# Kernel tuning notes

Hardware: AMD Instinct MI355X
Metric: run time of the kernel (lower is better)

Reference implementation:

```python
import jax, jax.numpy as jnp
import numpy as np

B, T, C, N = 4, 12, 64, 10000
H = 64            # d_inner (GRU hidden)
L = 2             # num_layers
NE = 2000         # number of static hyperedges
NNZ = 80000       # incidence list length
TOPK = 10         # HGCNADP_topk
DE = 16           # HGCNADP_embed_dims
RATE = 0.5        # hyperedge_rate (blend static vs adaptive)


def setup_inputs() -> dict:
    key = jax.random.key(0)
    ks = jax.random.split(key, 10)
    scale = 0.05
    x = jax.random.normal(ks[0], (B, T, C, N), jnp.float32)
    node_idx = jax.random.randint(ks[1], (NNZ,), 0, N, jnp.int32)
    edge_idx = jax.random.randint(ks[2], (NNZ,), 0, NE, jnp.int32)
    hyperedge_index = jnp.stack([node_idx, edge_idx])  # (2, NNZ)
    node_embs = jax.random.normal(ks[3], (L, N, DE), jnp.float32) * 0.1
    W_zr = jax.random.normal(ks[4], (L, C + H, 2 * H), jnp.float32) * scale
    b_zr = jnp.zeros((L, 2 * H), jnp.float32)
    W_c = jax.random.normal(ks[5], (L, C + H, H), jnp.float32) * scale
    b_c = jnp.zeros((L, H), jnp.float32)
    W_out = jax.random.normal(ks[6], (L, H, C), jnp.float32) * scale
    b_out = jnp.zeros((L, C), jnp.float32)
    return {"x": x, "hyperedge_index": hyperedge_index, "node_embs": node_embs,
            "W_zr": W_zr, "b_zr": b_zr, "W_c": W_c, "b_c": b_c,
            "W_out": W_out, "b_out": b_out}


def reference(x, hyperedge_index, node_embs, W_zr, b_zr, W_c, b_c, W_out, b_out):
    # x: (B, T, C, N). Dropout is identity (eval mode).
    node_idx = hyperedge_index[0]
    edge_idx = hyperedge_index[1]
    edge_deg = jnp.zeros((NE,), x.dtype).at[edge_idx].add(1.0)
    inv_e = 1.0 / jnp.maximum(edge_deg, 1.0)
    node_deg = jnp.zeros((N,), x.dtype).at[node_idx].add(1.0)
    inv_n = 1.0 / jnp.maximum(node_deg, 1.0)

    def conv(f, topk_idx, topk_w):
        # f: (B, N, D). Static hypergraph pass: node -> hyperedge -> node.
        msg = jnp.take(f, node_idx, axis=1)                       # (B, NNZ, D)
        eagg = jnp.zeros((f.shape[0], NE, f.shape[2]), f.dtype).at[:, edge_idx].add(msg)
        eagg = eagg * inv_e[None, :, None]                        # (B, NE, D)
        stat = jnp.zeros_like(f).at[:, node_idx].add(jnp.take(eagg, edge_idx, axis=1))
        stat = stat * inv_n[None, :, None]                        # (B, N, D)
        # Adaptive top-k hyperedge aggregation (softmax-weighted neighbor sum).
        adp = jnp.einsum('bnkd,nk->bnd', jnp.take(f, topk_idx, axis=1), topk_w)
        return RATE * stat + (1.0 - RATE) * adp

    out = x
    for l in range(L):
        xl = out.transpose(0, 1, 3, 2)                            # (B, T, N, C)
        E = node_embs[l]
        scores = jax.nn.relu(E @ E.T)                             # (N, N)
        vals, idx = jax.lax.top_k(scores, TOPK)                   # (N, K)
        w = jax.nn.softmax(vals, axis=-1)
        Wz, bz = W_zr[l], b_zr[l]
        Wc_, bc_ = W_c[l], b_c[l]
        Wo, bo = W_out[l], b_out[l]

        def step(h, x_t):
            zr = jax.nn.sigmoid(conv(jnp.concatenate([x_t, h], -1), idx, w) @ Wz + bz)
            z, r = jnp.split(zr, 2, axis=-1)
            c = jnp.tanh(conv(jnp.concatenate([x_t, r * h], -1), idx, w) @ Wc_ + bc_)
            h_new = z * h + (1.0 - z) * c
            return h_new, h_new @ Wo + bo

        h0 = jnp.zeros((out.shape[0], N, H), x.dtype)
        _, ys = jax.lax.scan(step, h0, xl.transpose(1, 0, 2, 3))  # ys: (T, B, N, C)
        out = out + ys.transpose(1, 0, 3, 2)                      # residual, back to (B,T,C,N)
    return out
```

## Files before the change

kernel.cpp:

```cpp
#include <hip/hip_runtime.h>
#include <hip/hip_fp16.h>
#include <cstdio>

#define BB 4
#define TT 12
#define CC 64
#define NN 10000
#define HH 64
#define LL 2
#define NEDGE 2000
#define NNZT 80000
#define KTOP 10
#define DEMB 16
#define BT (BB*TT)
#define TOPK_BLKS 1250
#define TRN_BLKS 30048

typedef long long ll;
typedef unsigned long long u64;
typedef unsigned int u32;
typedef unsigned short ushort;

typedef short bf16x8 __attribute__((ext_vector_type(8)));
typedef float f32x4 __attribute__((ext_vector_type(4)));

__device__ __forceinline__ void up8(const uint4 v, float* f) {
  const __half2* p = reinterpret_cast<const __half2*>(&v);
  float2 t0 = __half22float2(p[0]);
  float2 t1 = __half22float2(p[1]);
  float2 t2 = __half22float2(p[2]);
  float2 t3 = __half22float2(p[3]);
  f[0]=t0.x; f[1]=t0.y; f[2]=t1.x; f[3]=t1.y;
  f[4]=t2.x; f[5]=t2.y; f[6]=t3.x; f[7]=t3.y;
}
__device__ __forceinline__ uint4 pk8(const float* f) {
  __half2 h0 = __floats2half2_rn(f[0], f[1]);
  __half2 h1 = __floats2half2_rn(f[2], f[3]);
  __half2 h2 = __floats2half2_rn(f[4], f[5]);
  __half2 h3 = __floats2half2_rn(f[6], f[7]);
  uint4 r;
  r.x = *reinterpret_cast<unsigned*>(&h0);
  r.y = *reinterpret_cast<unsigned*>(&h1);
  r.z = *reinterpret_cast<unsigned*>(&h2);
  r.w = *reinterpret_cast<unsigned*>(&h3);
  return r;
}
__device__ __forceinline__ ushort f2bf(float x) {
  u32 u = __float_as_uint(x);
  u32 r = u + 0x7FFFu + ((u >> 16) & 1u);
  return (ushort)(r >> 16);
}
__device__ __forceinline__ uint4 pk8bf(const float* f) {
  uint4 r;
  r.x = (u32)f2bf(f[0]) | ((u32)f2bf(f[1])<<16);
  r.y = (u32)f2bf(f[2]) | ((u32)f2bf(f[3])<<16);
  r.z = (u32)f2bf(f[4]) | ((u32)f2bf(f[5])<<16);
  r.w = (u32)f2bf(f[6]) | ((u32)f2bf(f[7])<<16);
  return r;
}

__global__ void deg_kernel(const int* __restrict__ nidx, const int* __restrict__ eidx,
                           int* __restrict__ ndeg, int* __restrict__ edeg) {
  int i = blockIdx.x*256 + threadIdx.x;
  if (i < NNZT) { atomicAdd(&ndeg[nidx[i]],1); atomicAdd(&edeg[eidx[i]],1); }
}

__global__ void exscan_kernel(const int* __restrict__ cnt, int* __restrict__ off, int n) {
  __shared__ int part[256];
  int tid = threadIdx.x;
  int chunk = (n + 255)/256;
  int lo = tid*chunk, hi = min(lo+chunk, n);
  int s = 0;
  for (int i=lo; i<hi; ++i) s += cnt[i];
  part[tid]=s; __syncthreads();
  if (tid==0){ int acc=0; for(int i=0;i<256;++i){int v=part[i];part[i]=acc;acc+=v;} off[n]=acc; }
  __syncthreads();
  int acc = part[tid];
  for (int i=lo; i<hi; ++i){ off[i]=acc; acc+=cnt[i]; }
}

__global__ void fill_csr_kernel(const int* __restrict__ nidx, const int* __restrict__ eidx,
                                const int* __restrict__ noff, const int* __restrict__ eoff,
                                int* __restrict__ ncur, int* __restrict__ ecur,
                                int* __restrict__ node_edges, int* __restrict__ edge_nodes) {
  int i = blockIdx.x*256 + threadIdx.x;
  if (i >= NNZT) return;
  int n = nidx[i], e = eidx[i];
  int pn = atomicAdd(&ncur[n],1);
  node_edges[noff[n]+pn] = e;
  int pe = atomicAdd(&ecur[e],1);
  edge_nodes[eoff[e]+pe] = n;
}

__global__ void invdeg_kernel(const int* __restrict__ ndeg, const int* __restrict__ edeg,
                              float* __restrict__ inv_n, float* __restrict__ inv_e) {
  int i = blockIdx.x*256+threadIdx.x;
  if (i < NN) inv_n[i] = 1.0f/fmaxf((float)ndeg[i],1.0f);
  if (i < NEDGE) inv_e[i] = 1.0f/fmaxf((float)edeg[i],1.0f);
}

__global__ void prep_w_kernel(const float* __restrict__ W_zr, const float* __restrict__ W_c,
                              const float* __restrict__ W_o,
                              short* __restrict__ Wz_swb, short* __restrict__ Wc_swb,
                              short* __restrict__ Wo_swb) {
  int l = blockIdx.y;
  const float* Wz = W_zr + (size_t)l*128*128;
  const float* Wc = W_c  + (size_t)l*128*64;
  const float* Wo = W_o  + (size_t)l*64*64;
  short* Wz_sw = Wz_swb + (size_t)l*16384;
  short* Wc_sw = Wc_swb + (size_t)l*8192;
  short* Wo_sw = Wo_swb + (size_t)l*4096;
  int idx = blockIdx.x*256 + threadIdx.x;
  if (idx < 16384) {
    int i = idx&7, lane = (idx>>3)&63, kk = (idx>>9)&3, tc = idx>>11;
    int k = kk*32 + (lane>>4)*8 + i, col = tc*16 + (lane&15);
    Wz_sw[idx] = (short)f2bf(Wz[k*128+col]);
  }
  if (idx < 8192) {
    int i = idx&7, lane = (idx>>3)&63, kk = (idx>>9)&3, tc = idx>>11;
    int k = kk*32 + (lane>>4)*8 + i, col = tc*16 + (lane&15);
    Wc_sw[idx] = (short)f2bf(Wc[k*64+col]);
  }
  if (idx < 4096) {
    int i = idx&7, lane = (idx>>3)&63, kk = (idx>>9)&1, tc = idx>>10;
    int k = kk*32 + (lane>>4)*8 + i, col = tc*16 + (lane&15);
    Wo_sw[idx] = (short)f2bf(Wo[k*64+col]);
  }
}

__device__ __forceinline__ u64 sortstep(u64 X, int j, bool dir, int lane) {
  u64 p = __shfl_xor(X, j);
  bool lower = ((lane & j) == 0);
  bool keep_min = (dir == lower);
  bool xlt = (X < p);
  u64 mn = xlt ? X : p;
  u64 mx = xlt ? p : X;
  return keep_min ? mn : mx;
}

__device__ __forceinline__ void reselect(u64* bq, u64& thr, int& cnt, int lane) {
  int tot = 10 + cnt;
  u64 A = (lane < tot)      ? bq[lane]      : 0ull;
  u64 B = (lane + 64 < tot) ? bq[lane + 64] : 0ull;
  for (int k = 2; k <= 32; k <<= 1) {
    for (int j = k >> 1; j >= 1; j >>= 1) {
      bool dir = ((lane & k) == 0);
      A = sortstep(A, j, dir, lane);
      B = sortstep(B, j, dir, lane);
    }
  }
  for (int j = 32; j >= 1; j >>= 1) {
    A = sortstep(A, j, true,  lane);
    B = sortstep(B, j, false, lane);
  }
  {
    bool lt = (A < B);
    u64 mn = lt ? A : B, mx = lt ? B : A;
    A = mn; B = mx;
  }
  for (int j = 32; j >= 1; j >>= 1) {
    A = sortstep(A, j, true, lane);
    B = sortstep(B, j, true, lane);
  }
  if (lane >= 54) bq[63 - lane] = B;
  thr = __shfl(B, 54);
  cnt = 0;
}

__device__ void topk_body(int layer, int qb, char* smem,
                          const float* __restrict__ embs, int2* __restrict__ tkc_b) {
  u64 (*buf)[128] = (u64(*)[128])smem;
  const float* E = embs + (ll)layer*NN*DEMB;
  int2* tkc = tkc_b + (ll)layer*NN*KTOP;
  int tid = threadIdx.x;
  int wv = tid >> 6, lane = tid & 63;
  int qbase = qb*16 + wv*4;
  const float4* E4 = (const float4*)E;
  float4 q[4][4];
  #pragma unroll
  for (int u=0;u<4;++u) {
    int n = qbase + u;
    #pragma unroll
    for (int j=0;j<4;++j) q[u][j] = E4[(ll)n*4 + j];
  }
  u64 thr[4] = {0,0,0,0};
  float thrf[4] = {0.f,0.f,0.f,0.f};
  int cnt[4] = {0,0,0,0};
  buf[tid>>4][tid&15] = 0ull;
  for (int cb=0; cb<NN; cb+=64) {
    int cand = cb + lane;
    bool valid = (cand < NN);
    int ca = valid ? cand : 0;
    float4 a0 = E4[(ll)ca*4], a1 = E4[(ll)ca*4+1], a2 = E4[(ll)ca*4+2], a3 = E4[(ll)ca*4+3];
    u64 low = (u64)(0x00FFFFFFu - (unsigned)cand);
    float sv[4];
    #pragma unroll
    for (int u=0;u<4;++u) {
      float dot = q[u][0].x*a0.x + q[u][0].y*a0.y + q[u][0].z*a0.z + q[u][0].w*a0.w
                + q[u][1].x*a1.x + q[u][1].y*a1.y + q[u][1].z*a1.z + q[u][1].w*a1.w
                + q[u][2].x*a2.x + q[u][2].y*a2.y + q[u][2].z*a2.z + q[u][2].w*a2.w
                + q[u][3].x*a3.x + q[u][3].y*a3.y + q[u][3].z*a3.z + q[u][3].w*a3.w;
      float s = fmaxf(dot, 0.f);
      sv[u] = valid ? s : -1.f;
    }
    #pragma unroll
    for (int u=0;u<4;++u) {
      u64 mask = __ballot(sv[u] >= thrf[u]);
      if (mask) {
        if (sv[u] >= thrf[u]) {
          u64 key = ((u64)__float_as_uint(sv[u]) << 32) | low;
          int myofs = (int)__popcll(mask & ((1ull<<lane)-1ull));
          buf[wv*4+u][10 + cnt[u] + myofs] = key;
        }
        cnt[u] += (int)__popcll(mask);
        if (cnt[u] >= 40) {
          reselect(&buf[wv*4+u][0], thr[u], cnt[u], lane);
          thrf[u] = __uint_as_float((u32)(thr[u] >> 32));
        }
      }
    }
  }
  #pragma unroll
  for (int u=0;u<4;++u) {
    u64* bq = &buf[wv*4+u][0];
    if (cnt[u] > 0) reselect(bq, thr[u], cnt[u], lane);
    u64 k10 = (lane < 10) ? bq[lane] : 0ull;
    float v = __uint_as_float((unsigned)(k10 >> 32));
    int idx = 0x00FFFFFF - (int)(k10 & 0xFFFFFFFFull);
    float v0 = __shfl(v, 0);
    float e = (lane < 10) ? expf(v - v0) : 0.f;
    float s = e;
    for (int o=1;o<16;o<<=1) s += __shfl_xor(s, o);
    if (lane < 10) {
      int n = qbase + u;
      tkc[n*KTOP + lane] = make_int2(idx, __float_as_int(e / s));
    }
  }
}

__device__ void transpose_body(int tb, char* smem,
                               const float* __restrict__ src, __half* __restrict__ dst) {
  float (*tile)[33] = (float(*)[33])smem;
  int tid = threadIdx.x;
  int tx = tid & 31, ty = tid >> 5;
  int bt = tb / 626;
  int rem = tb % 626;
  int n0 = (rem % 313)*32, c0 = (rem/313)*32;
  for (int i=ty; i<32; i+=8) {
    int c = c0+i, nn = n0+tx;
    tile[i][tx] = (nn<NN)? src[((ll)bt*CC + c)*NN + nn] : 0.0f;
  }
  __syncthreads();
  for (int i=ty; i<32; i+=8) {
    int nn = n0+i, c = c0+tx;
    if (nn<NN) dst[((ll)bt*NN+nn)*64 + c] = __float2half_rn(tile[tx][i]);
  }
}

__global__ void __launch_bounds__(256) mega1_kernel(const float* __restrict__ embs,
                                                    int2* __restrict__ tkc,
                                                    const float* __restrict__ x,
                                                    __half* __restrict__ xt) {
  __shared__ __align__(16) char smem[16384];
  int bid = blockIdx.x;
  if (bid < TOPK_BLKS) topk_body(bid/625, bid%625, smem, embs, tkc);
  else transpose_body(bid - TOPK_BLKS, smem, x, xt);
}

__global__ void transpose_kernel(const float* __restrict__ src, __half* __restrict__ dst) {
  __shared__ __align__(16) char smem[4352];
  int tb = (blockIdx.z*626) + blockIdx.y*313 + blockIdx.x;
  transpose_body(tb, smem, src, dst);
}

__global__ void __launch_bounds__(256) edge_agg_kernel(
    const uint4* __restrict__ f8, uint4* __restrict__ eagg8,
    const int* __restrict__ eoff, const int* __restrict__ enodes,
    const float* __restrict__ inv_e) {
  __shared__ int en_s[1088];
  __shared__ int jo_s[17];
  int tid = threadIdx.x;
  int e0 = blockIdx.x*16;
  int s = blockIdx.y;
  if (tid < 17) jo_s[tid] = eoff[e0 + tid];
  __syncthreads();
  int jb0 = jo_s[0], cnt = jo_s[16] - jb0;
  bool stg = (cnt <= 1088);
  if (stg) for (int i = tid; i < cnt; i += 256) en_s[i] = enodes[jb0 + i];
  __syncthreads();
  int esub = tid>>4;
  int e = e0 + esub;
  int hsel = (tid>>3)&1;
  int lane8 = tid&7;
  int j0 = jo_s[esub] - jb0, j1 = jo_s[esub+1] - jb0;
  const uint4* fb = f8 + (ll)s*NN*8;
  float acc[8] = {0,0,0,0,0,0,0,0};
  for (int j = j0 + hsel; j < j1; j += 2) {
    int node = stg ? en_s[j] : enodes[jb0+j];
    float t[8]; up8(fb[(ll)node*8 + lane8], t);
    #pragma unroll
    for (int q=0;q<8;++q) acc[q] += t[q];
  }
  #pragma unroll
  for (int q=0;q<8;++q) acc[q] += __shfl_xor(acc[q], 8);
  if (hsel == 0) {
    float sc = inv_e[e];
    #pragma unroll
    for (int q=0;q<8;++q) acc[q] *= sc;
    eagg8[((ll)s*NEDGE+e)*8 + lane8] = pk8(acc);
  }
}

__global__ void __launch_bounds__(256) conv_x_kernel(
    const uint4* __restrict__ xt8, const uint4* __restrict__ eagg8,
    const int* __restrict__ noff, const int* __restrict__ nedges,
    const float* __restrict__ inv_n,
    const int2* __restrict__ tkc,
    uint4* __restrict__ cx8) {
  __shared__ int tki_s[32][KTOP];
  __shared__ float tkw_s[32][KTOP];
  __shared__ int ne_s[640];
  __shared__ int no_s[33];
  int tid = threadIdx.x; int s = blockIdx.y; int n0 = blockIdx.x*32;
  if (tid < 33) no_s[tid] = noff[min(n0 + tid, NN)];
  for (int i=tid; i<32*KTOP; i+=256) {
    int r=i/KTOP, k=i%KTOP; int n = n0+r;
    int2 p = (n<NN)? tkc[n*KTOP+k] : make_int2(0,0);
    tki_s[r][k] = p.x;
    tkw_s[r][k] = __int_as_float(p.y);
  }
  __syncthreads();
  int jb0 = no_s[0], cnt = no_s[32] - jb0;
  bool stg = (cnt <= 640);
  if (stg) for (int i=tid; i<cnt; i+=256) ne_s[i] = nedges[jb0+i];
  __syncthreads();
  int row = tid>>3, lane8 = tid&7;
  int n = n0 + row;
  if (n >= NN) return;
  float stv[8] = {0,0,0,0,0,0,0,0};
  const uint4* eb = eagg8 + (ll)s*NEDGE*8;
  int j0 = no_s[row] - jb0, j1 = no_s[row+1] - jb0;
  for (int j=j0;j<j1;++j) {
    int eidx = stg ? ne_s[j] : nedges[jb0+j];
    float t[8]; up8(eb[(ll)eidx*8 + lane8], t);
    #pragma unroll
    for (int q=0;q<8;++q) stv[q] += t[q];
  }
  float sc = 0.5f*inv_n[n];
  float adv[8] = {0,0,0,0,0,0,0,0};
  const uint4* xb = xt8 + (ll)s*NN*8;
  #pragma unroll
  for (int k=0;k<KTOP;++k) {
    float w = tkw_s[row][k];
    float t[8]; up8(xb[(ll)tki_s[row][k]*8 + lane8], t);
    #pragma unroll
    for (int q=0;q<8;++q) adv[q] += w*t[q];
  }
  float r8[8];
  #pragma unroll
  for (int q=0;q<8;++q) r8[q] = sc*stv[q] + 0.5f*adv[q];
  cx8[((ll)s*NN+n)*8+lane8] = pk8bf(r8);
}

__global__ void __launch_bounds__(256) step0_kernel(
    const uint4* __restrict__ cx8,
    const short* __restrict__ Wz_sw, const float* __restrict__ bz,
    const short* __restrict__ Wc_sw, const float* __restrict__ bc,
    const short* __restrict__ Wo_sw, const float* __restrict__ bo,
    __half* __restrict__ h, float* __restrict__ out) {
  __shared__ __align__(16) short in_bf[32][72];
  __shared__ __align__(16) short hn[32][72];
  __shared__ __align__(16) float yt[64][36];
  int tid = threadIdx.x;
  int b = blockIdx.y; int n0 = blockIdx.x*32;
  int bt = b*TT;
  {
    int row = tid>>3, lane8 = tid&7;
    int n = n0 + row;
    uint4 cxv4 = make_uint4(0,0,0,0);
    if (n < NN) cxv4 = cx8[((ll)bt*NN + n)*8 + lane8];
    *(uint4*)&in_bf[row][lane8*8] = cxv4;
  }
  __syncthreads();
  int wv = tid>>6, lane = tid&63;
  int m = lane&15, g = lane>>4;
  #pragma unroll
  for (int q=0;q<2;++q) {
    int T = wv + 4*q;
    int tr = T>>2, tc = T&3;
    f32x4 az = {0.f,0.f,0.f,0.f};
    f32x4 ac = {0.f,0.f,0.f,0.f};
    #pragma unroll
    for (int kk=0;kk<2;++kk) {
      bf16x8 a = *(const bf16x8*)&in_bf[tr*16 + m][kk*32 + g*8];
      bf16x8 bwz = *(const bf16x8*)&Wz_sw[((tc*4+kk)*64 + lane)*8];
      bf16x8 bwc = *(const bf16x8*)&Wc_sw[((tc*4+kk)*64 + lane)*8];
      az = __builtin_amdgcn_mfma_f32_16x16x32_bf16(a, bwz, az, 0, 0, 0);
      ac = __builtin_amdgcn_mfma_f32_16x16x32_bf16(a, bwc, ac, 0, 0, 0);
    }
    int col = tc*16 + m;
    float bzv = bz[col], bcv = bc[col];
    #pragma unroll
    for (int r=0;r<4;++r) {
      int row = tr*16 + g*4 + r;
      int n = n0 + row;
      float z = 1.0f/(1.0f+expf(-(az[r]+bzv)));
      float cval = tanhf(ac[r]+bcv);
      float hnew = (1.0f-z)*cval;
      if (n < NN) h[((ll)b*NN+n)*64+col] = __float2half_rn(hnew);
      hn[row][col] = (short)f2bf(hnew);
    }
  }
  __syncthreads();
  #pragma unroll
  for (int q=0;q<2;++q) {
    int T = wv + 4*q;
    int tr = T>>2, tc = T&3;
    f32x4 acc = {0.f,0.f,0.f,0.f};
    #pragma unroll
    for (int kk=0;kk<2;++kk) {
      bf16x8 a = *(const bf16x8*)&hn[tr*16 + m][kk*32 + g*8];
      bf16x8 bw = *(const bf16x8*)&Wo_sw[((tc*2+kk)*64 + lane)*8];
      acc = __builtin_amdgcn_mfma_f32_16x16x32_bf16(a, bw, acc, 0, 0, 0);
    }
    int col = tc*16 + m;
    float bias = bo[col];
    #pragma unroll
    for (int r=0;r<4;++r) {
      int row = tr*16 + g*4 + r;
      yt[col][row] = acc[r] + bias;
    }
  }
  __syncthreads();
  #pragma unroll
  for (int kk=0;kk<2;++kk) {
    int slot = tid + kk*256;
    int col = slot>>3, q = slot&7;
    int n = n0 + q*4;
    if (n < NN) {
      float4 y = *(const float4*)&yt[col][q*4];
      float4* dst = (float4*)&out[((ll)bt*64+col)*NN + n];
      float4 cur = *dst;
      cur.x += y.x; cur.y += y.y; cur.z += y.z; cur.w += y.w;
      *dst = cur;
    }
  }
}

__global__ void __launch_bounds__(256) step_zr_kernel(
    const uint4* __restrict__ h8, const uint4* __restrict__ cx8,
    const uint4* __restrict__ eagg8,
    const short* __restrict__ Wz_sw, const float* __restrict__ bz,
    const int* __restrict__ noff, const int* __restrict__ nedges,
    const float* __restrict__ inv_n,
    const int2* __restrict__ tkc,
    const __half* __restrict__ hs,
    __half* __restrict__ rh, __half* __restrict__ zout, int t) {
  __shared__ __align__(16) short in_bf[32][136];
  __shared__ int tki_s[32][KTOP];
  __shared__ float tkw_s[32][KTOP];
  __shared__ int ne_s[640];
  __shared__ int no_s[33];
  int tid = threadIdx.x;
  int b = blockIdx.y; int n0 = blockIdx.x*32;
  int bt = b*TT + t;
  if (tid < 33) no_s[tid] = noff[min(n0 + tid, NN)];
  for (int i=tid; i<32*KTOP; i+=256) {
    int r=i/KTOP, k=i%KTOP; int n=n0+r;
    int2 p = (n<NN)? tkc[n*KTOP+k] : make_int2(0,0);
    tki_s[r][k] = p.x;
    tkw_s[r][k] = __int_as_float(p.y);
  }
  __syncthreads();
  int jb0 = no_s[0], ecnt = no_s[32] - jb0;
  bool stg = (ecnt <= 640);
  if (stg) for (int i=tid; i<ecnt; i+=256) ne_s[i] = nedges[jb0+i];
  __syncthreads();
  {
    int row = tid>>3, lane8 = tid&7;
    int n = n0 + row;
    uint4 cxv4 = make_uint4(0,0,0,0);
    float chv[8] = {0,0,0,0,0,0,0,0};
    if (n < NN) {
      cxv4 = cx8[((ll)bt*NN + n)*8 + lane8];
      float stv[8] = {0,0,0,0,0,0,0,0};
      int j0 = no_s[row] - jb0, j1 = no_s[row+1] - jb0;
      const uint4* eb = eagg8 + (ll)b*NEDGE*8;
      for (int j=j0;j<j1;++j) {
        int eidx = stg ? ne_s[j] : nedges[jb0+j];
        float t8[8]; up8(eb[(ll)eidx*8 + lane8], t8);
        #pragma unroll
        for (int q=0;q<8;++q) stv[q] += t8[q];
      }
      float sc = 0.5f*inv_n[n];
      const uint4* hb = h8 + (ll)b*NN*8;
      float adv[8] = {0,0,0,0,0,0,0,0};
      #pragma unroll
      for (int k=0;k<KTOP;++k) {
        float w = tkw_s[row][k];
        float t8[8]; up8(hb[(ll)tki_s[row][k]*8 + lane8], t8);
        #pragma unroll
        for (int q=0;q<8;++q) adv[q] += w*t8[q];
      }
      #pragma unroll
      for (int q=0;q<8;++q) chv[q] = sc*stv[q] + 0.5f*adv[q];
    }
    *(uint4*)&in_bf[row][lane8*8]    = cxv4;
    *(uint4*)&in_bf[row][64+lane8*8] = pk8bf(chv);
  }
  __syncthreads();
  int wv = tid>>6, lane = tid&63;
  int m = lane&15, g = lane>>4;
  #pragma unroll
  for (int q=0;q<4;++q) {
    int T = wv*4 + q;
    int tr = T>>3, tc = T&7;
    f32x4 acc = {0.f,0.f,0.f,0.f};
    #pragma unroll
    for (int kk=0;kk<4;++kk) {
      bf16x8 a = *(const bf16x8*)&in_bf[tr*16 + m][kk*32 + g*8];
      bf16x8 bf = *(const bf16x8*)&Wz_sw[((tc*4+kk)*64 + lane)*8];
      acc = __builtin_amdgcn_mfma_f32_16x16x32_bf16(a, bf, acc, 0, 0, 0);
    }
    int col = tc*16 + m;
    float bias = bz[col];
    #pragma unroll
    for (int r=0;r<4;++r) {
      int row = tr*16 + g*4 + r;
      int n = n0 + row;
      if (n < NN) {
        float v = 1.0f/(1.0f+expf(-(acc[r]+bias)));
        if (col < 64) zout[((ll)b*NN+n)*64+col] = __float2half_rn(v);
        else {
          int c = col-64;
          float hv = __half2float(hs[((ll)b*NN+n)*64+c]);
          rh[((ll)b*NN+n)*64+c] = __float2half_rn(v*hv);
        }
      }
    }
  }
}

__global__ void __launch_bounds__(256) step_hy_kernel(
    const uint4* __restrict__ rh8, const uint4* __restrict__ cx8,
    const uint4* __restrict__ eagg8,
    const short* __restrict__ Wc_sw, const float* __restrict__ bc,
    const short* __restrict__ Wo_sw, const float* __restrict__ bo,
    const int* __restrict__ noff, const int* __restrict__ nedges,
    const float* __restrict__ inv_n,
    const int2* __restrict__ tkc,
    const __half* __restrict__ zbuf, __half* __restrict__ h,
    float* __restrict__ out, int t) {
  __shared__ __align__(16) short in_bf[32][136];
  __shared__ __align__(16) short hn[32][72];
  __shared__ __align__(16) float yt[64][36];
  __shared__ int tki_s[32][KTOP];
  __shared__ float tkw_s[32][KTOP];
  __shared__ int ne_s[640];
  __shared__ int no_s[33];
  int tid = threadIdx.x;
  int b = blockIdx.y; int n0 = blockIdx.x*32;
  int bt = b*TT + t;
  if (tid < 33) no_s[tid] = noff[min(n0 + tid, NN)];
  for (int i=tid; i<32*KTOP; i+=256) {
    int r=i/KTOP, k=i%KTOP; int n=n0+r;
    int2 p = (n<NN)? tkc[n*KTOP+k] : make_int2(0,0);
    tki_s[r][k] = p.x;
    tkw_s[r][k] = __int_as_float(p.y);
  }
  __syncthreads();
  int jb0 = no_s[0], ecnt = no_s[32] - jb0;
  bool stg = (ecnt <= 640);
  if (stg) for (int i=tid; i<ecnt; i+=256) ne_s[i] = nedges[jb0+i];
  __syncthreads();
  {
    int row = tid>>3, lane8 = tid&7;
    int n = n0 + row;
    uint4 cxv4 = make_uint4(0,0,0,0);
    float chv[8] = {0,0,0,0,0,0,0,0};
    if (n < NN) {
      cxv4 = cx8[((ll)bt*NN + n)*8 + lane8];
      float stv[8] = {0,0,0,0,0,0,0,0};
      int j0 = no_s[row] - jb0, j1 = no_s[row+1] - jb0;
      const uint4* eb = eagg8 + (ll)b*NEDGE*8;
      for (int j=j0;j<j1;++j) {
        int eidx = stg ? ne_s[j] : nedges[jb0+j];
        float t8[8]; up8(eb[(ll)eidx*8 + lane8], t8);
        #pragma unroll
        for (int q=0;q<8;++q) stv[q] += t8[q];
      }
      float sc = 0.5f*inv_n[n];
      const uint4* rb = rh8 + (ll)b*NN*8;
      float adv[8] = {0,0,0,0,0,0,0,0};
      #pragma unroll
      for (int k=0;k<KTOP;++k) {
        float w = tkw_s[row][k];
        float t8[8]; up8(rb[(ll)tki_s[row][k]*8 + lane8], t8);
        #pragma unroll
        for (int q=0;q<8;++q) adv[q] += w*t8[q];
      }
      #pragma unroll
      for (int q=0;q<8;++q) chv[q] = sc*stv[q] + 0.5f*adv[q];
    }
    *(uint4*)&in_bf[row][lane8*8]    = cxv4;
    *(uint4*)&in_bf[row][64+lane8*8] = pk8bf(chv);
  }
  __syncthreads();
  int wv = tid>>6, lane = tid&63;
  int m = lane&15, g = lane>>4;
  #pragma unroll
  for (int q=0;q<2;++q) {
    int T = wv + 4*q;
    int tr = T>>2, tc = T&3;
    f32x4 acc = {0.f,0.f,0.f,0.f};
    #pragma unroll
    for (int kk=0;kk<4;++kk) {
      bf16x8 a = *(const bf16x8*)&in_bf[tr*16 + m][kk*32 + g*8];
      bf16x8 bf = *(const bf16x8*)&Wc_sw[((tc*4+kk)*64 + lane)*8];
      acc = __builtin_amdgcn_mfma_f32_16x16x32_bf16(a, bf, acc, 0, 0, 0);
    }
    int col = tc*16 + m;
    float bias = bc[col];
    #pragma unroll
    for (int r=0;r<4;++r) {
      int row = tr*16 + g*4 + r;
      int n = n0 + row;
      float hnew = 0.0f;
      if (n < NN) {
        float cval = tanhf(acc[r]+bias);
        float z = __half2float(zbuf[((ll)b*NN+n)*64+col]);
        float hv = __half2float(h[((ll)b*NN+n)*64+col]);
        hnew = z*hv + (1.0f-z)*cval;
        h[((ll)b*NN+n)*64+col] = __float2half_rn(hnew);
      }
      hn[row][col] = (short)f2bf(hnew);
    }
  }
  __syncthreads();
  #pragma unroll
  for (int q=0;q<2;++q) {
    int T = wv + 4*q;
    int tr = T>>2, tc = T&3;
    f32x4 acc = {0.f,0.f,0.f,0.f};
    #pragma unroll
    for (int kk=0;kk<2;++kk) {
      bf16x8 a = *(const bf16x8*)&hn[tr*16 + m][kk*32 + g*8];
      bf16x8 bf = *(const bf16x8*)&Wo_sw[((tc*2+kk)*64 + lane)*8];
      acc = __builtin_amdgcn_mfma_f32_16x16x32_bf16(a, bf, acc, 0, 0, 0);
    }
    int col = tc*16 + m;
    float bias = bo[col];
    #pragma unroll
    for (int r=0;r<4;++r) {
      int row = tr*16 + g*4 + r;
      yt[col][row] = acc[r] + bias;
    }
  }
  __syncthreads();
  #pragma unroll
  for (int kk=0;kk<2;++kk) {
    int slot = tid + kk*256;
    int col = slot>>3, q = slot&7;
    int n = n0 + q*4;
    if (n < NN) {
      float4 y = *(const float4*)&yt[col][q*4];
      float4* dst = (float4*)&out[((ll)bt*64+col)*NN + n];
      float4 cur = *dst;
      cur.x += y.x; cur.y += y.y; cur.z += y.z; cur.w += y.w;
      *dst = cur;
    }
  }
}

extern "C" void kernel_launch(void* const* d_in, const int* in_sizes, int n_in,
                              void* d_out, int out_size, void* d_ws, size_t ws_size,
                              hipStream_t stream) {
  const float* x    = (const float*)d_in[0];
  const int*  hidx  = (const int*)d_in[1];
  const float* embs = (const float*)d_in[2];
  const float* W_zr = (const float*)d_in[3];
  const float* b_zr = (const float*)d_in[4];
  const float* W_c  = (const float*)d_in[5];
  const float* b_c  = (const float*)d_in[6];
  const float* W_out= (const float*)d_in[7];
  const float* b_out= (const float*)d_in[8];
  const int* node_idx = hidx;
  const int* edge_idx = hidx + NNZT;

  char* ws = (char*)d_ws;
  size_t off = 0;
  auto alloc = [&](size_t bytes) -> void* {
    void* p = ws + off; off += (bytes + 255) & ~(size_t)255; return p;
  };
  __half* xt    = (__half*)alloc((size_t)BT*NN*64*2);
  __half* cx    = (__half*)alloc((size_t)BT*NN*64*2);
  __half* eaggx = (__half*)alloc((size_t)BT*NEDGE*64*2);
  __half* eaggh = (__half*)alloc((size_t)BB*NEDGE*64*2);
  __half* hbuf  = (__half*)alloc((size_t)BB*NN*64*2);
  __half* rhbuf = (__half*)alloc((size_t)BB*NN*64*2);
  __half* zbuf  = (__half*)alloc((size_t)BB*NN*64*2);
  short* Wz_sw = (short*)alloc((size_t)LL*16384*2);
  short* Wc_sw = (short*)alloc((size_t)LL*8192*2);
  short* Wo_sw = (short*)alloc((size_t)LL*4096*2);
  int2* tkc    = (int2*)alloc((size_t)LL*NN*KTOP*8);
  float* inv_e = (float*)alloc(NEDGE*4);
  float* inv_n = (float*)alloc(NN*4);
  int* ndeg    = (int*)alloc(NN*4);
  int* edeg    = (int*)alloc(NEDGE*4);
  int* noff    = (int*)alloc((NN+1)*4);
  int* eoff    = (int*)alloc((NEDGE+1)*4);
  int* ncur    = (int*)alloc(NN*4);
  int* ecur    = (int*)alloc(NEDGE*4);
  int* nedges  = (int*)alloc(NNZT*4);
  int* enodes  = (int*)alloc(NNZT*4);
  if (off > ws_size) {
    fprintf(stderr, "kernel_launch: ws too small, need %zu have %zu\n", off, ws_size);
    return;
  }

  hipMemcpyAsync(d_out, x, (size_t)BB*TT*CC*NN*4, hipMemcpyDeviceToDevice, stream);

  hipMemsetAsync(ndeg, 0, NN*4, stream);
  hipMemsetAsync(edeg, 0, NEDGE*4, stream);
  hipMemsetAsync(ncur, 0, NN*4, stream);
  hipMemsetAsync(ecur, 0, NEDGE*4, stream);
  deg_kernel<<<(NNZT+255)/256,256,0,stream>>>(node_idx, edge_idx, ndeg, edeg);
  exscan_kernel<<<1,256,0,stream>>>(ndeg, noff, NN);
  exscan_kernel<<<1,256,0,stream>>>(edeg, eoff, NEDGE);
  fill_csr_kernel<<<(NNZT+255)/256,256,0,stream>>>(node_idx, edge_idx, noff, eoff,
                                                   ncur, ecur, nedges, enodes);
  invdeg_kernel<<<(NN+255)/256,256,0,stream>>>(ndeg, edeg, inv_n, inv_e);

  prep_w_kernel<<<dim3(64,LL),256,0,stream>>>(W_zr, W_c, W_out, Wz_sw, Wc_sw, Wo_sw);
  float* outp = (float*)d_out;
  mega1_kernel<<<TOPK_BLKS + TRN_BLKS,256,0,stream>>>(embs, tkc, outp, xt);

  for (int l=0; l<LL; ++l) {
    const short* Wzs = Wz_sw + (size_t)l*16384;
    const short* Wcs = Wc_sw + (size_t)l*8192;
    const short* Wos = Wo_sw + (size_t)l*4096;
    const float* bz = b_zr + l*128;
    const float* bc = b_c + l*64;
    const float* bo = b_out + l*64;
    const int2* tkcl = tkc + (size_t)l*NN*KTOP;
    if (l > 0)
      transpose_kernel<<<dim3(313, 2, BT), 256, 0, stream>>>(outp, xt);
    edge_agg_kernel<<<dim3(125, BT),256,0,stream>>>(
        (const uint4*)xt, (uint4*)eaggx, eoff, enodes, inv_e);
    conv_x_kernel<<<dim3(313, BT),256,0,stream>>>(
        (const uint4*)xt, (const uint4*)eaggx, noff, nedges, inv_n, tkcl, (uint4*)cx);
    step0_kernel<<<dim3(313, BB),256,0,stream>>>(
        (const uint4*)cx, Wzs, bz, Wcs, bc, Wos, bo, hbuf, outp);
    for (int t=1; t<TT; ++t) {
      edge_agg_kernel<<<dim3(125, BB),256,0,stream>>>(
          (const uint4*)hbuf, (uint4*)eaggh, eoff, enodes, inv_e);
      step_zr_kernel<<<dim3(313, BB),256,0,stream>>>(
          (const uint4*)hbuf, (const uint4*)cx, (const uint4*)eaggh, Wzs, bz,
          noff, nedges, inv_n, tkcl, hbuf, rhbuf, zbuf, t);
      edge_agg_kernel<<<dim3(125, BB),256,0,stream>>>(
          (const uint4*)rhbuf, (uint4*)eaggh, eoff, enodes, inv_e);
      step_hy_kernel<<<dim3(313, BB),256,0,stream>>>(
          (const uint4*)rhbuf, (const uint4*)cx, (const uint4*)eaggh, Wcs, bc, Wos, bo,
          noff, nedges, inv_n, tkcl, zbuf, hbuf, outp, t);
    }
  }
}
```

Baseline: 2.354 ms.

## Halve node tile in recurrent step kernels and split edge aggregation finer

The per-timestep GRU kernels (step0, step_zr, step_hy) now process 16 nodes per block instead of 32, doubling the grid to 625 blocks per batch. This exposes more parallelism in the small B=4 recurrent launches, and since 10000 is divisible by 16 the bounds checks can be dropped. A new edge aggregation kernel handles 8 edges per block with 4 partial sums per edge, used for the hidden-state passes, to raise occupancy. The top-k scan also prefetches the next candidate embeddings one iteration ahead to hide load latency. In exchange, only half the threads do the gather work in the step kernels, and the per-edge reduction needs an extra shuffle.

```diff
diff --git a/kernel.cpp b/kernel.cpp
--- a/kernel.cpp
+++ b/kernel.cpp
@@ -15,6 +15,7 @@
 #define BT (BB*TT)
 #define TOPK_BLKS 1250
 #define TRN_BLKS 30048
+#define NB16 625
 
 typedef long long ll;
 typedef unsigned long long u64;
@@ -187,11 +188,21 @@
   float thrf[4] = {0.f,0.f,0.f,0.f};
   int cnt[4] = {0,0,0,0};
   buf[tid>>4][tid&15] = 0ull;
+  float4 a0,a1,a2,a3;
+  {
+    int ca = (lane < NN) ? lane : 0;
+    a0=E4[(ll)ca*4]; a1=E4[(ll)ca*4+1]; a2=E4[(ll)ca*4+2]; a3=E4[(ll)ca*4+3];
+  }
   for (int cb=0; cb<NN; cb+=64) {
+    float4 b0,b1,b2,b3;
+    int ncb = cb + 64;
+    if (ncb < NN) {
+      int cand2 = ncb + lane;
+      int ca2 = (cand2 < NN) ? cand2 : 0;
+      b0=E4[(ll)ca2*4]; b1=E4[(ll)ca2*4+1]; b2=E4[(ll)ca2*4+2]; b3=E4[(ll)ca2*4+3];
+    }
     int cand = cb + lane;
     bool valid = (cand < NN);
-    int ca = valid ? cand : 0;
-    float4 a0 = E4[(ll)ca*4], a1 = E4[(ll)ca*4+1], a2 = E4[(ll)ca*4+2], a3 = E4[(ll)ca*4+3];
     u64 low = (u64)(0x00FFFFFFu - (unsigned)cand);
     float sv[4];
     #pragma unroll
@@ -219,6 +230,7 @@
         }
       }
     }
+    a0=b0; a1=b1; a2=b2; a3=b3;
   }
   #pragma unroll
   for (int u=0;u<4;++u) {
@@ -304,6 +316,46 @@
   #pragma unroll
   for (int q=0;q<8;++q) acc[q] += __shfl_xor(acc[q], 8);
   if (hsel == 0) {
+    float sc = inv_e[e];
+    #pragma unroll
+    for (int q=0;q<8;++q) acc[q] *= sc;
+    eagg8[((ll)s*NEDGE+e)*8 + lane8] = pk8(acc);
+  }
+}
+
+__global__ void __launch_bounds__(256) edge_agg8_kernel(
+    const uint4* __restrict__ f8, uint4* __restrict__ eagg8,
+    const int* __restrict__ eoff, const int* __restrict__ enodes,
+    const float* __restrict__ inv_e) {
+  __shared__ int en_s[576];
+  __shared__ int jo_s[9];
+  int tid = threadIdx.x;
+  int e0 = blockIdx.x*8;
+  int s = blockIdx.y;
+  if (tid < 9) jo_s[tid] = eoff[e0 + tid];
+  __syncthreads();
+  int jb0 = jo_s[0], cnt = jo_s[8] - jb0;
+  bool stg = (cnt <= 576);
+  if (stg) for (int i = tid; i < cnt; i += 256) en_s[i] = enodes[jb0 + i];
+  __syncthreads();
+  int esub = tid>>5;
+  int e = e0 + esub;
+  int sub = (tid>>3)&3;
+  int lane8 = tid&7;
+  int j0 = jo_s[esub] - jb0, j1 = jo_s[esub+1] - jb0;
+  const uint4* fb = f8 + (ll)s*NN*8;
+  float acc[8] = {0,0,0,0,0,0,0,0};
+  for (int j = j0 + sub; j < j1; j += 4) {
+    int node = stg ? en_s[j] : enodes[jb0+j];
+    float t[8]; up8(fb[(ll)node*8 + lane8], t);
+    #pragma unroll
+    for (int q=0;q<8;++q) acc[q] += t[q];
+  }
+  #pragma unroll
+  for (int q=0;q<8;++q) acc[q] += __shfl_xor(acc[q], 8);
+  #pragma unroll
+  for (int q=0;q<8;++q) acc[q] += __shfl_xor(acc[q], 16);
+  if (sub == 0) {
     float sc = inv_e[e];
     #pragma unroll
     for (int q=0;q<8;++q) acc[q] *= sc;
@@ -368,31 +420,27 @@
     const short* __restrict__ Wc_sw, const float* __restrict__ bc,
     const short* __restrict__ Wo_sw, const float* __restrict__ bo,
     __half* __restrict__ h, float* __restrict__ out) {
-  __shared__ __align__(16) short in_bf[32][72];
-  __shared__ __align__(16) short hn[32][72];
-  __shared__ __align__(16) float yt[64][36];
+  __shared__ __align__(16) short in_bf[16][72];
+  __shared__ __align__(16) short hn[16][72];
+  __shared__ __align__(16) float yt[64][20];
   int tid = threadIdx.x;
-  int b = blockIdx.y; int n0 = blockIdx.x*32;
+  int b = blockIdx.y; int n0 = blockIdx.x*16;
   int bt = b*TT;
-  {
+  if (tid < 128) {
     int row = tid>>3, lane8 = tid&7;
     int n = n0 + row;
-    uint4 cxv4 = make_uint4(0,0,0,0);
-    if (n < NN) cxv4 = cx8[((ll)bt*NN + n)*8 + lane8];
-    *(uint4*)&in_bf[row][lane8*8] = cxv4;
+    *(uint4*)&in_bf[row][lane8*8] = cx8[((ll)bt*NN + n)*8 + lane8];
   }
   __syncthreads();
   int wv = tid>>6, lane = tid&63;
   int m = lane&15, g = lane>>4;
-  #pragma unroll
-  for (int q=0;q<2;++q) {
-    int T = wv + 4*q;
-    int tr = T>>2, tc = T&3;
+  {
+    int tc = wv;
     f32x4 az = {0.f,0.f,0.f,0.f};
     f32x4 ac = {0.f,0.f,0.f,0.f};
     #pragma unroll
     for (int kk=0;kk<2;++kk) {
-      bf16x8 a = *(const bf16x8*)&in_bf[tr*16 + m][kk*32 + g*8];
+      bf16x8 a = *(const bf16x8*)&in_bf[m][kk*32 + g*8];
       bf16x8 bwz = *(const bf16x8*)&Wz_sw[((tc*4+kk)*64 + lane)*8];
       bf16x8 bwc = *(const bf16x8*)&Wc_sw[((tc*4+kk)*64 + lane)*8];
       az = __builtin_amdgcn_mfma_f32_16x16x32_bf16(a, bwz, az, 0, 0, 0);
@@ -402,48 +450,39 @@
     float bzv = bz[col], bcv = bc[col];
     #pragma unroll
     for (int r=0;r<4;++r) {
-      int row = tr*16 + g*4 + r;
+      int row = g*4 + r;
       int n = n0 + row;
       float z = 1.0f/(1.0f+expf(-(az[r]+bzv)));
       float cval = tanhf(ac[r]+bcv);
       float hnew = (1.0f-z)*cval;
-      if (n < NN) h[((ll)b*NN+n)*64+col] = __float2half_rn(hnew);
+      h[((ll)b*NN+n)*64+col] = __float2half_rn(hnew);
       hn[row][col] = (short)f2bf(hnew);
     }
   }
   __syncthreads();
-  #pragma unroll
-  for (int q=0;q<2;++q) {
-    int T = wv + 4*q;
-    int tr = T>>2, tc = T&3;
+  {
+    int tc = wv;
     f32x4 acc = {0.f,0.f,0.f,0.f};
     #pragma unroll
     for (int kk=0;kk<2;++kk) {
-      bf16x8 a = *(const bf16x8*)&hn[tr*16 + m][kk*32 + g*8];
+      bf16x8 a = *(const bf16x8*)&hn[m][kk*32 + g*8];
       bf16x8 bw = *(const bf16x8*)&Wo_sw[((tc*2+kk)*64 + lane)*8];
       acc = __builtin_amdgcn_mfma_f32_16x16x32_bf16(a, bw, acc, 0, 0, 0);
     }
     int col = tc*16 + m;
     float bias = bo[col];
     #pragma unroll
-    for (int r=0;r<4;++r) {
-      int row = tr*16 + g*4 + r;
-      yt[col][row] = acc[r] + bias;
-    }
-  }
-  __syncthreads();
-  #pragma unroll
-  for (int kk=0;kk<2;++kk) {
-    int slot = tid + kk*256;
-    int col = slot>>3, q = slot&7;
+    for (int r=0;r<4;++r) yt[col][g*4 + r] = acc[r] + bias;
+  }
+  __syncthreads();
+  {
+    int col = tid>>2, q = tid&3;
     int n = n0 + q*4;
-    if (n < NN) {
-      float4 y = *(const float4*)&yt[col][q*4];
-      float4* dst = (float4*)&out[((ll)bt*64+col)*NN + n];
-      float4 cur = *dst;
-      cur.x += y.x; cur.y += y.y; cur.z += y.z; cur.w += y.w;
-      *dst = cur;
-    }
+    float4 y = *(const float4*)&yt[col][q*4];
+    float4* dst = (float4*)&out[((ll)bt*64+col)*NN + n];
+    float4 cur = *dst;
+    cur.x += y.x; cur.y += y.y; cur.z += y.z; cur.w += y.w;
+    *dst = cur;
   }
 }
 
@@ -456,55 +495,52 @@
     const int2* __restrict__ tkc,
     const __half* __restrict__ hs,
     __half* __restrict__ rh, __half* __restrict__ zout, int t) {
-  __shared__ __align__(16) short in_bf[32][136];
-  __shared__ int tki_s[32][KTOP];
-  __shared__ float tkw_s[32][KTOP];
-  __shared__ int ne_s[640];
-  __shared__ int no_s[33];
+  __shared__ __align__(16) short in_bf[16][136];
+  __shared__ int tki_s[16][KTOP];
+  __shared__ float tkw_s[16][KTOP];
+  __shared__ int ne_s[384];
+  __shared__ int no_s[17];
   int tid = threadIdx.x;
-  int b = blockIdx.y; int n0 = blockIdx.x*32;
+  int b = blockIdx.y; int n0 = blockIdx.x*16;
   int bt = b*TT + t;
-  if (tid < 33) no_s[tid] = noff[min(n0 + tid, NN)];
-  for (int i=tid; i<32*KTOP; i+=256) {
-    int r=i/KTOP, k=i%KTOP; int n=n0+r;
-    int2 p = (n<NN)? tkc[n*KTOP+k] : make_int2(0,0);
+  if (tid < 17) no_s[tid] = noff[n0 + tid];
+  for (int i=tid; i<16*KTOP; i+=256) {
+    int r=i/KTOP, k=i%KTOP;
+    int2 p = tkc[(n0+r)*KTOP+k];
     tki_s[r][k] = p.x;
     tkw_s[r][k] = __int_as_float(p.y);
   }
   __syncthreads();
-  int jb0 = no_s[0], ecnt = no_s[32] - jb0;
-  bool stg = (ecnt <= 640);
+  int jb0 = no_s[0], ecnt = no_s[16] - jb0;
+  bool stg = (ecnt <= 384);
   if (stg) for (int i=tid; i<ecnt; i+=256) ne_s[i] = nedges[jb0+i];
   __syncthreads();
-  {
+  if (tid < 128) {
     int row = tid>>3, lane8 = tid&7;
     int n = n0 + row;
-    uint4 cxv4 = make_uint4(0,0,0,0);
-    float chv[8] = {0,0,0,0,0,0,0,0};
-    if (n < NN) {
-      cxv4 = cx8[((ll)bt*NN + n)*8 + lane8];
-      float stv[8] = {0,0,0,0,0,0,0,0};
-      int j0 = no_s[row] - jb0, j1 = no_s[row+1] - jb0;
-      const uint4* eb = eagg8 + (ll)b*NEDGE*8;
-      for (int j=j0;j<j1;++j) {
-        int eidx = stg ? ne_s[j] : nedges[jb0+j];
-        float t8[8]; up8(eb[(ll)eidx*8 + lane8], t8);
-        #pragma unroll
-        for (int q=0;q<8;++q) stv[q] += t8[q];
-      }
-      float sc = 0.5f*inv_n[n];
-      const uint4* hb = h8 + (ll)b*NN*8;
-      float adv[8] = {0,0,0,0,0,0,0,0};
+    uint4 cxv4 = cx8[((ll)bt*NN + n)*8 + lane8];
+    float stv[8] = {0,0,0,0,0,0,0,0};
+    int j0 = no_s[row] - jb0, j1 = no_s[row+1] - jb0;
+    const uint4* eb = eagg8 + (ll)b*NEDGE*8;
+    for (int j=j0;j<j1;++j) {
+      int eidx = stg ? ne_s[j] : nedges[jb0+j];
+      float t8[8]; up8(eb[(ll)eidx*8 + lane8], t8);
       #pragma unroll
-      for (int k=0;k<KTOP;++k) {
-        float w = tkw_s[row][k];
-        float t8[8]; up8(hb[(ll)tki_s[row][k]*8 + lane8], t8);
-        #pragma unroll
-        for (int q=0;q<8;++q) adv[q] += w*t8[q];
-      }
+      for (int q=0;q<8;++q) stv[q] += t8[q];
+    }
+    float sc = 0.5f*inv_n[n];
+    const uint4* hb = h8 + (ll)b*NN*8;
+    float adv[8] = {0,0,0,0,0,0,0,0};
+    #pragma unroll
+    for (int k=0;k<KTOP;++k) {
+      float w = tkw_s[row][k];
+      float t8[8]; up8(hb[(ll)tki_s[row][k]*8 + lane8], t8);
       #pragma unroll
-      for (int q=0;q<8;++q) chv[q] = sc*stv[q] + 0.5f*adv[q];
-    }
+      for (int q=0;q<8;++q) adv[q] += w*t8[q];
+    }
+    float chv[8];
+    #pragma unroll
+    for (int q=0;q<8;++q) chv[q] = sc*stv[q] + 0.5f*adv[q];
     *(uint4*)&in_bf[row][lane8*8]    = cxv4;
     *(uint4*)&in_bf[row][64+lane8*8] = pk8bf(chv);
   }
@@ -512,13 +548,12 @@
   int wv = tid>>6, lane = tid&63;
   int m = lane&15, g = lane>>4;
   #pragma unroll
-  for (int q=0;q<4;++q) {
-    int T = wv*4 + q;
-    int tr = T>>3, tc = T&7;
+  for (int q=0;q<2;++q) {
+    int tc = wv + 4*q;
     f32x4 acc = {0.f,0.f,0.f,0.f};
     #pragma unroll
     for (int kk=0;kk<4;++kk) {
-      bf16x8 a = *(const bf16x8*)&in_bf[tr*16 + m][kk*32 + g*8];
+      bf16x8 a = *(const bf16x8*)&in_bf[m][kk*32 + g*8];
       bf16x8 bf = *(const bf16x8*)&Wz_sw[((tc*4+kk)*64 + lane)*8];
       acc = __builtin_amdgcn_mfma_f32_16x16x32_bf16(a, bf, acc, 0, 0, 0);
     }
@@ -526,16 +561,14 @@
     float bias = bz[col];
     #pragma unroll
     for (int r=0;r<4;++r) {
-      int row = tr*16 + g*4 + r;
+      int row = g*4 + r;
       int n = n0 + row;
-      if (n < NN) {
-        float v = 1.0f/(1.0f+expf(-(acc[r]+bias)));
-        if (col < 64) zout[((ll)b*NN+n)*64+col] = __float2half_rn(v);
-        else {
-          int c = col-64;
-          float hv = __half2float(hs[((ll)b*NN+n)*64+c]);
-          rh[((ll)b*NN+n)*64+c] = __float2half_rn(v*hv);
-        }
+      float v = 1.0f/(1.0f+expf(-(acc[r]+bias)));
+      if (col < 64) zout[((ll)b*NN+n)*64+col] = __float2half_rn(v);
+      else {
+        int c = col-64;
+        float hv = __half2float(hs[((ll)b*NN+n)*64+c]);
+        rh[((ll)b*NN+n)*64+c] = __float2half_rn(v*hv);
       }
     }
   }
@@ -551,71 +584,66 @@
     const int2* __restrict__ tkc,
     const __half* __restrict__ zbuf, __half* __restrict__ h,
     float* __restrict__ out, int t) {
-  __shared__ __align__(16) short in_bf[32][136];
-  __shared__ __align__(16) short hn[32][72];
-  __shared__ __align__(16) float yt[64][36];
-  __shared__ int tki_s[32][KTOP];
-  __shared__ float tkw_s[32][KTOP];
-  __shared__ int ne_s[640];
-  __shared__ int no_s[33];
+  __shared__ __align__(16) short in_bf[16][136];
+  __shared__ __align__(16) short hn[16][72];
+  __shared__ __align__(16) float yt[64][20];
+  __shared__ int tki_s[16][KTOP];
+  __shared__ float tkw_s[16][KTOP];
+  __shared__ int ne_s[384];
+  __shared__ int no_s[17];
   int tid = threadIdx.x;
-  int b = blockIdx.y; int n0 = blockIdx.x*32;
+  int b = blockIdx.y; int n0 = blockIdx.x*16;
   int bt = b*TT + t;
-  if (tid < 33) no_s[tid] = noff[min(n0 + tid, NN)];
-  for (int i=tid; i<32*KTOP; i+=256) {
-    int r=i/KTOP, k=i%KTOP; int n=n0+r;
-    int2 p = (n<NN)? tkc[n*KTOP+k] : make_int2(0,0);
+  if (tid < 17) no_s[tid] = noff[n0 + tid];
+  for (int i=tid; i<16*KTOP; i+=256) {
+    int r=i/KTOP, k=i%KTOP;
+    int2 p = tkc[(n0+r)*KTOP+k];
     tki_s[r][k] = p.x;
     tkw_s[r][k] = __int_as_float(p.y);
   }
   __syncthreads();
-  int jb0 = no_s[0], ecnt = no_s[32] - jb0;
-  bool stg = (ecnt <= 640);
+  int jb0 = no_s[0], ecnt = no_s[16] - jb0;
+  bool stg = (ecnt <= 384);
   if (stg) for (int i=tid; i<ecnt; i+=256) ne_s[i] = nedges[jb0+i];
   __syncthreads();
-  {
+  if (tid < 128) {
     int row = tid>>3, lane8 = tid&7;
     int n = n0 + row;
-    uint4 cxv4 = make_uint4(0,0,0,0);
-    float chv[8] = {0,0,0,0,0,0,0,0};
-    if (n < NN) {
-      cxv4 = cx8[((ll)bt*NN + n)*8 + lane8];
-      float stv[8] = {0,0,0,0,0,0,0,0};
-      int j0 = no_s[row] - jb0, j1 = no_s[row+1] - jb0;
-      const uint4* eb = eagg8 + (ll)b*NEDGE*8;
-      for (int j=j0;j<j1;++j) {
-        int eidx = stg ? ne_s[j] : nedges[jb0+j];
-        float t8[8]; up8(eb[(ll)eidx*8 + lane8], t8);
-        #pragma unroll
-        for (int q=0;q<8;++q) stv[q] += t8[q];
-      }
-      float sc = 0.5f*inv_n[n];
-      const uint4* rb = rh8 + (ll)b*NN*8;
-      float adv[8] = {0,0,0,0,0,0,0,0};
+    uint4 cxv4 = cx8[((ll)bt*NN + n)*8 + lane8];
+    float stv[8] = {0,0,0,0,0,0,0,0};
+    int j0 = no_s[row] - jb0, j1 = no_s[row+1] - jb0;
+    const uint4* eb = eagg8 + (ll)b*NEDGE*8;
+    for (int j=j0;j<j1;++j) {
+      int eidx = stg ? ne_s[j] : nedges[jb0+j];
+      float t8[8]; up8(eb[(ll)eidx*8 + lane8], t8);
       #pragma unroll
-      for (int k=0;k<KTOP;++k) {
-        float w = tkw_s[row][k];
-        float t8[8]; up8(rb[(ll)tki_s[row][k]*8 + lane8], t8);
-        #pragma unroll
-        for (int q=0;q<8;++q) adv[q] += w*t8[q];
-      }
+      for (int q=0;q<8;++q) stv[q] += t8[q];
+    }
+    float sc = 0.5f*inv_n[n];
+    const uint4* rb = rh8 + (ll)b*NN*8;
+    float adv[8] = {0,0,0,0,0,0,0,0};
+    #pragma unroll
+    for (int k=0;k<KTOP;++k) {
+      float w = tkw_s[row][k];
+      float t8[8]; up8(rb[(ll)tki_s[row][k]*8 + lane8], t8);
       #pragma unroll
-      for (int q=0;q<8;++q) chv[q] = sc*stv[q] + 0.5f*adv[q];
-    }
+      for (int q=0;q<8;++q) adv[q] += w*t8[q];
+    }
+    float chv[8];
+    #pragma unroll
+    for (int q=0;q<8;++q) chv[q] = sc*stv[q] + 0.5f*adv[q];
     *(uint4*)&in_bf[row][lane8*8]    = cxv4;
     *(uint4*)&in_bf[row][64+lane8*8] = pk8bf(chv);
   }
   __syncthreads();
   int wv = tid>>6, lane = tid&63;
   int m = lane&15, g = lane>>4;
-  #pragma unroll
-  for (int q=0;q<2;++q) {
-    int T = wv + 4*q;
-    int tr = T>>2, tc = T&3;
+  {
+    int tc = wv;
     f32x4 acc = {0.f,0.f,0.f,0.f};
     #pragma unroll
     for (int kk=0;kk<4;++kk) {
-      bf16x8 a = *(const bf16x8*)&in_bf[tr*16 + m][kk*32 + g*8];
+      bf16x8 a = *(const bf16x8*)&in_bf[m][kk*32 + g*8];
       bf16x8 bf = *(const bf16x8*)&Wc_sw[((tc*4+kk)*64 + lane)*8];
       acc = __builtin_amdgcn_mfma_f32_16x16x32_bf16(a, bf, acc, 0, 0, 0);
     }
@@ -623,52 +651,40 @@
     float bias = bc[col];
     #pragma unroll
     for (int r=0;r<4;++r) {
-      int row = tr*16 + g*4 + r;
+      int row = g*4 + r;
       int n = n0 + row;
-      float hnew = 0.0f;
-      if (n < NN) {
-        float cval = tanhf(acc[r]+bias);
-        float z = __half2float(zbuf[((ll)b*NN+n)*64+col]);
-        float hv = __half2float(h[((ll)b*NN+n)*64+col]);
-        hnew = z*hv + (1.0f-z)*cval;
-        h[((ll)b*NN+n)*64+col] = __float2half_rn(hnew);
-      }
+      float cval = tanhf(acc[r]+bias);
+      float z = __half2float(zbuf[((ll)b*NN+n)*64+col]);
+      float hv = __half2float(h[((ll)b*NN+n)*64+col]);
+      float hnew = z*hv + (1.0f-z)*cval;
+      h[((ll)b*NN+n)*64+col] = __float2half_rn(hnew);
       hn[row][col] = (short)f2bf(hnew);
     }
   }
   __syncthreads();
-  #pragma unroll
-  for (int q=0;q<2;++q) {
-    int T = wv + 4*q;
-    int tr = T>>2, tc = T&3;
+  {
+    int tc = wv;
     f32x4 acc = {0.f,0.f,0.f,0.f};
     #pragma unroll
     for (int kk=0;kk<2;++kk) {
-      bf16x8 a = *(const bf16x8*)&hn[tr*16 + m][kk*32 + g*8];
+      bf16x8 a = *(const bf16x8*)&hn[m][kk*32 + g*8];
       bf16x8 bf = *(const bf16x8*)&Wo_sw[((tc*2+kk)*64 + lane)*8];
       acc = __builtin_amdgcn_mfma_f32_16x16x32_bf16(a, bf, acc, 0, 0, 0);
     }
     int col = tc*16 + m;
     float bias = bo[col];
     #pragma unroll
-    for (int r=0;r<4;++r) {
-      int row = tr*16 + g*4 + r;
-      yt[col][row] = acc[r] + bias;
-    }
-  }
-  __syncthreads();
-  #pragma unroll
-  for (int kk=0;kk<2;++kk) {
-    int slot = tid + kk*256;
-    int col = slot>>3, q = slot&7;
+    for (int r=0;r<4;++r) yt[col][g*4 + r] = acc[r] + bias;
+  }
+  __syncthreads();
+  {
+    int col = tid>>2, q = tid&3;
     int n = n0 + q*4;
-    if (n < NN) {
-      float4 y = *(const float4*)&yt[col][q*4];
-      float4* dst = (float4*)&out[((ll)bt*64+col)*NN + n];
-      float4 cur = *dst;
-      cur.x += y.x; cur.y += y.y; cur.z += y.z; cur.w += y.w;
-      *dst = cur;
-    }
+    float4 y = *(const float4*)&yt[col][q*4];
+    float4* dst = (float4*)&out[((ll)bt*64+col)*NN + n];
+    float4 cur = *dst;
+    cur.x += y.x; cur.y += y.y; cur.z += y.z; cur.w += y.w;
+    *dst = cur;
   }
 }
 
@@ -749,17 +765,17 @@
         (const uint4*)xt, (uint4*)eaggx, eoff, enodes, inv_e);
     conv_x_kernel<<<dim3(313, BT),256,0,stream>>>(
         (const uint4*)xt, (const uint4*)eaggx, noff, nedges, inv_n, tkcl, (uint4*)cx);
-    step0_kernel<<<dim3(313, BB),256,0,stream>>>(
+    step0_kernel<<<dim3(NB16, BB),256,0,stream>>>(
         (const uint4*)cx, Wzs, bz, Wcs, bc, Wos, bo, hbuf, outp);
     for (int t=1; t<TT; ++t) {
-      edge_agg_kernel<<<dim3(125, BB),256,0,stream>>>(
+      edge_agg8_kernel<<<dim3(250, BB),256,0,stream>>>(
           (const uint4*)hbuf, (uint4*)eaggh, eoff, enodes, inv_e);
-      step_zr_kernel<<<dim3(313, BB),256,0,stream>>>(
+      step_zr_kernel<<<dim3(NB16, BB),256,0,stream>>>(
           (const uint4*)hbuf, (const uint4*)cx, (const uint4*)eaggh, Wzs, bz,
           noff, nedges, inv_n, tkcl, hbuf, rhbuf, zbuf, t);
-      edge_agg_kernel<<<dim3(125, BB),256,0,stream>>>(
+      edge_agg8_kernel<<<dim3(250, BB),256,0,stream>>>(
           (const uint4*)rhbuf, (uint4*)eaggh, eoff, enodes, inv_e);
-      step_hy_kernel<<<dim3(313, BB),256,0,stream>>>(
+      step_hy_kernel<<<dim3(NB16, BB),256,0,stream>>>(
           (const uint4*)rhbuf, (const uint4*)cx, (const uint4*)eaggh, Wcs, bc, Wos, bo,
           noff, nedges, inv_n, tkcl, zbuf, hbuf, outp, t);
     }
```

Measured after the change: 2.275 ms. 3.4% less time.
